# Kernel optimization log

Hardware: AMD Instinct MI355X
Metric: run time of the kernel (lower is better)

Reference implementation:

```python
import jax, jax.numpy as jnp
import numpy as np

B, S, H, E, TOP_K = 4, 4096, 4096, 64, 2

def setup_inputs() -> dict:
    key = jax.random.key(0)
    k1, k2 = jax.random.split(key)
    hidden_states = jax.random.normal(k1, (B, S, H), dtype=jnp.float32)
    gate_weight = jax.random.normal(k2, (E, H), dtype=jnp.float32) * (H ** -0.5)
    return {"hidden_states": hidden_states, "gate_weight": gate_weight}

def reference(hidden_states, gate_weight):
    # gate: logits[b,s,e] = hidden[b,s,h] @ W[e,h]^T (nn.Linear, no bias)
    router_logits = jnp.einsum('bsh,eh->bse', hidden_states, gate_weight)
    router_probs = jax.nn.softmax(router_logits, axis=-1)
    # top-k over experts, then renormalize the selected weights
    expert_weights, expert_indices = jax.lax.top_k(router_probs, TOP_K)
    expert_weights = expert_weights / jnp.sum(expert_weights, axis=-1, keepdims=True)
    return (router_probs, expert_indices, expert_weights)
```

## Files before the change

### kernel.cpp

```cpp
#include <hip/hip_runtime.h>
#include <math.h>

#define TOKENS 16384
#define HDIM 4096
#define NE 64

#define BM 128
#define BK 32
#define KSPLIT 8
#define KSLICE (HDIM / KSPLIT)

__global__ __launch_bounds__(128) void router_gemm(const float* __restrict__ A,
                                                   const float* __restrict__ W,
                                                   float* __restrict__ P) {
  __shared__ float As[BK][BM];
  __shared__ float Ws[BK][NE];

  const int tid = threadIdx.x;
  const int bt = blockIdx.x;
  const int ks = blockIdx.y;
  const int tx = tid & 7;
  const int ty = tid >> 3;

  const float* Ab = A + (size_t)(bt * BM + tid) * HDIM + (size_t)ks * KSLICE;
  const int we = tid >> 1;
  const int wk = (tid & 1) * 16;
  const float* Wb = W + (size_t)we * HDIM + (size_t)ks * KSLICE + wk;

  float acc[8][8];
#pragma unroll
  for (int i = 0; i < 8; ++i)
#pragma unroll
    for (int j = 0; j < 8; ++j) acc[i][j] = 0.f;

  for (int kc = 0; kc < KSLICE; kc += BK) {
#pragma unroll
    for (int i = 0; i < BK / 4; ++i) {
      float4 v = *(const float4*)(Ab + kc + i * 4);
      As[i * 4 + 0][tid] = v.x;
      As[i * 4 + 1][tid] = v.y;
      As[i * 4 + 2][tid] = v.z;
      As[i * 4 + 3][tid] = v.w;
    }
#pragma unroll
    for (int i = 0; i < 4; ++i) {
      float4 v = *(const float4*)(Wb + kc + i * 4);
      Ws[wk + i * 4 + 0][we] = v.x;
      Ws[wk + i * 4 + 1][we] = v.y;
      Ws[wk + i * 4 + 2][we] = v.z;
      Ws[wk + i * 4 + 3][we] = v.w;
    }
    __syncthreads();

#pragma unroll
    for (int k = 0; k < BK; ++k) {
      float a[8], w[8];
      *(float4*)&a[0] = *(const float4*)&As[k][ty * 8];
      *(float4*)&a[4] = *(const float4*)&As[k][ty * 8 + 4];
      *(float4*)&w[0] = *(const float4*)&Ws[k][tx * 8];
      *(float4*)&w[4] = *(const float4*)&Ws[k][tx * 8 + 4];
#pragma unroll
      for (int i = 0; i < 8; ++i)
#pragma unroll
        for (int j = 0; j < 8; ++j) acc[i][j] = fmaf(a[i], w[j], acc[i][j]);
    }
    __syncthreads();
  }

  float* Pb = P + ((size_t)ks * TOKENS + (size_t)bt * BM + ty * 8) * NE + tx * 8;
#pragma unroll
  for (int i = 0; i < 8; ++i) {
    float4 v0 = make_float4(acc[i][0], acc[i][1], acc[i][2], acc[i][3]);
    float4 v1 = make_float4(acc[i][4], acc[i][5], acc[i][6], acc[i][7]);
    *(float4*)(Pb + (size_t)i * NE) = v0;
    *(float4*)(Pb + (size_t)i * NE + 4) = v1;
  }
}

__global__ __launch_bounds__(64) void router_finalize(const float* __restrict__ P,
                                                      float* __restrict__ out) {
  const int tok = blockIdx.x * 64 + threadIdx.x;
  float l[NE];

#pragma unroll
  for (int j = 0; j < NE / 4; ++j) {
    float4 v = *(const float4*)(P + (size_t)tok * NE + j * 4);
    l[j * 4 + 0] = v.x; l[j * 4 + 1] = v.y; l[j * 4 + 2] = v.z; l[j * 4 + 3] = v.w;
  }
#pragma unroll
  for (int s = 1; s < KSPLIT; ++s) {
    const float* ps = P + ((size_t)s * TOKENS + tok) * NE;
#pragma unroll
    for (int j = 0; j < NE / 4; ++j) {
      float4 v = *(const float4*)(ps + j * 4);
      l[j * 4 + 0] += v.x; l[j * 4 + 1] += v.y; l[j * 4 + 2] += v.z; l[j * 4 + 3] += v.w;
    }
  }

  float m = l[0];
#pragma unroll
  for (int e = 1; e < NE; ++e) m = fmaxf(m, l[e]);
  float sum = 0.f;
#pragma unroll
  for (int e = 0; e < NE; ++e) { l[e] = expf(l[e] - m); sum += l[e]; }
  const float inv = 1.f / sum;

  float v0 = -1.f, v1 = -1.f;
  int i0 = 0, i1 = 0;
#pragma unroll
  for (int e = 0; e < NE; ++e) {
    float p = l[e] * inv;
    l[e] = p;
    if (p > v0) { v1 = v0; i1 = i0; v0 = p; i0 = e; }
    else if (p > v1) { v1 = p; i1 = e; }
  }

  float* probs = out + (size_t)tok * NE;
#pragma unroll
  for (int j = 0; j < NE / 4; ++j)
    *(float4*)(probs + j * 4) =
        make_float4(l[j * 4 + 0], l[j * 4 + 1], l[j * 4 + 2], l[j * 4 + 3]);

  float* idxo = out + (size_t)TOKENS * NE + (size_t)tok * 2;
  idxo[0] = (float)i0;
  idxo[1] = (float)i1;

  float* wo = out + (size_t)TOKENS * NE + (size_t)TOKENS * 2 + (size_t)tok * 2;
  const float rs = 1.f / (v0 + v1);
  wo[0] = v0 * rs;
  wo[1] = v1 * rs;
}

extern "C" void kernel_launch(void* const* d_in, const int* in_sizes, int n_in,
                              void* d_out, int out_size, void* d_ws, size_t ws_size,
                              hipStream_t stream) {
  const float* A = (const float*)d_in[0];
  const float* W = (const float*)d_in[1];
  float* out = (float*)d_out;
  float* P = (float*)d_ws;

  dim3 gridA(TOKENS / BM, KSPLIT);
  router_gemm<<<gridA, 128, 0, stream>>>(A, W, P);
  router_finalize<<<TOKENS / 64, 64, 0, stream>>>(P, out);
}
```

Baseline: 407.1 us.

## Retile router GEMM with register prefetch and wave-parallel softmax/top-k finalize

The GEMM moves from 128-token tiles with 8x8 per-thread outputs to 64-token tiles with 256 threads and 4x4 outputs. It pads the shared-memory arrays to reduce bank conflicts and prefetches the next K chunk into registers while the current one is computed. The finalize kernel changes from one thread per token to one wavefront per token, doing max, sum and top-2 with shuffles and ballots instead of serial loops over 64 registers. The aim is more parallelism and lower latency, at the cost of lower arithmetic intensity per thread and more LDS traffic per FMA in the GEMM.

```diff
diff --git a/kernel.cpp b/kernel.cpp
--- a/kernel.cpp
+++ b/kernel.cpp
@@ -5,130 +5,134 @@
 #define HDIM 4096
 #define NE 64
 
-#define BM 128
+#define BM 64
 #define BK 32
 #define KSPLIT 8
 #define KSLICE (HDIM / KSPLIT)
+#define LDSP 68
 
-__global__ __launch_bounds__(128) void router_gemm(const float* __restrict__ A,
-                                                   const float* __restrict__ W,
-                                                   float* __restrict__ P) {
-  __shared__ float As[BK][BM];
-  __shared__ float Ws[BK][NE];
+__global__ __launch_bounds__(256, 4) void router_gemm(const float* __restrict__ A,
+                                                      const float* __restrict__ W,
+                                                      float* __restrict__ P) {
+  __shared__ float As[BK * LDSP];
+  __shared__ float Ws[BK * LDSP];
 
   const int tid = threadIdx.x;
   const int bt = blockIdx.x;
   const int ks = blockIdx.y;
-  const int tx = tid & 7;
-  const int ty = tid >> 3;
 
-  const float* Ab = A + (size_t)(bt * BM + tid) * HDIM + (size_t)ks * KSLICE;
-  const int we = tid >> 1;
-  const int wk = (tid & 1) * 16;
-  const float* Wb = W + (size_t)we * HDIM + (size_t)ks * KSLICE + wk;
+  const int sr = tid >> 2;
+  const int sc = (tid & 3) * 4;
 
-  float acc[8][8];
+  const float* Ab = A + (size_t)(bt * BM + sr) * HDIM + (size_t)ks * KSLICE + sc;
+  const float* Wb = W + (size_t)sr * HDIM + (size_t)ks * KSLICE + sc;
+
+  const int tx = tid & 15;
+  const int ty = tid >> 4;
+
+  float acc[4][4];
 #pragma unroll
-  for (int i = 0; i < 8; ++i)
+  for (int i = 0; i < 4; ++i)
 #pragma unroll
-    for (int j = 0; j < 8; ++j) acc[i][j] = 0.f;
+    for (int j = 0; j < 4; ++j) acc[i][j] = 0.f;
+
+  float4 a0 = *(const float4*)(Ab);
+  float4 a1 = *(const float4*)(Ab + 16);
+  float4 w0 = *(const float4*)(Wb);
+  float4 w1 = *(const float4*)(Wb + 16);
 
   for (int kc = 0; kc < KSLICE; kc += BK) {
-#pragma unroll
-    for (int i = 0; i < BK / 4; ++i) {
-      float4 v = *(const float4*)(Ab + kc + i * 4);
-      As[i * 4 + 0][tid] = v.x;
-      As[i * 4 + 1][tid] = v.y;
-      As[i * 4 + 2][tid] = v.z;
-      As[i * 4 + 3][tid] = v.w;
+    As[(sc + 0) * LDSP + sr] = a0.x;
+    As[(sc + 1) * LDSP + sr] = a0.y;
+    As[(sc + 2) * LDSP + sr] = a0.z;
+    As[(sc + 3) * LDSP + sr] = a0.w;
+    As[(sc + 16) * LDSP + sr] = a1.x;
+    As[(sc + 17) * LDSP + sr] = a1.y;
+    As[(sc + 18) * LDSP + sr] = a1.z;
+    As[(sc + 19) * LDSP + sr] = a1.w;
+    Ws[(sc + 0) * LDSP + sr] = w0.x;
+    Ws[(sc + 1) * LDSP + sr] = w0.y;
+    Ws[(sc + 2) * LDSP + sr] = w0.z;
+    Ws[(sc + 3) * LDSP + sr] = w0.w;
+    Ws[(sc + 16) * LDSP + sr] = w1.x;
+    Ws[(sc + 17) * LDSP + sr] = w1.y;
+    Ws[(sc + 18) * LDSP + sr] = w1.z;
+    Ws[(sc + 19) * LDSP + sr] = w1.w;
+    __syncthreads();
+
+    if (kc + BK < KSLICE) {
+      a0 = *(const float4*)(Ab + kc + BK);
+      a1 = *(const float4*)(Ab + kc + BK + 16);
+      w0 = *(const float4*)(Wb + kc + BK);
+      w1 = *(const float4*)(Wb + kc + BK + 16);
     }
-#pragma unroll
-    for (int i = 0; i < 4; ++i) {
-      float4 v = *(const float4*)(Wb + kc + i * 4);
-      Ws[wk + i * 4 + 0][we] = v.x;
-      Ws[wk + i * 4 + 1][we] = v.y;
-      Ws[wk + i * 4 + 2][we] = v.z;
-      Ws[wk + i * 4 + 3][we] = v.w;
-    }
-    __syncthreads();
 
 #pragma unroll
     for (int k = 0; k < BK; ++k) {
-      float a[8], w[8];
-      *(float4*)&a[0] = *(const float4*)&As[k][ty * 8];
-      *(float4*)&a[4] = *(const float4*)&As[k][ty * 8 + 4];
-      *(float4*)&w[0] = *(const float4*)&Ws[k][tx * 8];
-      *(float4*)&w[4] = *(const float4*)&Ws[k][tx * 8 + 4];
+      float4 av = *(const float4*)&As[k * LDSP + ty * 4];
+      float4 wv = *(const float4*)&Ws[k * LDSP + tx * 4];
+      const float a[4] = {av.x, av.y, av.z, av.w};
+      const float w[4] = {wv.x, wv.y, wv.z, wv.w};
 #pragma unroll
-      for (int i = 0; i < 8; ++i)
+      for (int i = 0; i < 4; ++i)
 #pragma unroll
-        for (int j = 0; j < 8; ++j) acc[i][j] = fmaf(a[i], w[j], acc[i][j]);
+        for (int j = 0; j < 4; ++j) acc[i][j] = fmaf(a[i], w[j], acc[i][j]);
     }
     __syncthreads();
   }
 
-  float* Pb = P + ((size_t)ks * TOKENS + (size_t)bt * BM + ty * 8) * NE + tx * 8;
+  float* Pb = P + ((size_t)ks * TOKENS + (size_t)bt * BM + ty * 4) * NE + tx * 4;
 #pragma unroll
-  for (int i = 0; i < 8; ++i) {
-    float4 v0 = make_float4(acc[i][0], acc[i][1], acc[i][2], acc[i][3]);
-    float4 v1 = make_float4(acc[i][4], acc[i][5], acc[i][6], acc[i][7]);
-    *(float4*)(Pb + (size_t)i * NE) = v0;
-    *(float4*)(Pb + (size_t)i * NE + 4) = v1;
-  }
+  for (int i = 0; i < 4; ++i)
+    *(float4*)(Pb + (size_t)i * NE) =
+        make_float4(acc[i][0], acc[i][1], acc[i][2], acc[i][3]);
 }
 
-__global__ __launch_bounds__(64) void router_finalize(const float* __restrict__ P,
-                                                      float* __restrict__ out) {
-  const int tok = blockIdx.x * 64 + threadIdx.x;
-  float l[NE];
+__global__ __launch_bounds__(256) void router_finalize(const float* __restrict__ P,
+                                                       float* __restrict__ out) {
+  const int lane = threadIdx.x & 63;
+  const int wave = threadIdx.x >> 6;
+  const int tok = blockIdx.x * 4 + wave;
 
+  float l = 0.f;
 #pragma unroll
-  for (int j = 0; j < NE / 4; ++j) {
-    float4 v = *(const float4*)(P + (size_t)tok * NE + j * 4);
-    l[j * 4 + 0] = v.x; l[j * 4 + 1] = v.y; l[j * 4 + 2] = v.z; l[j * 4 + 3] = v.w;
+  for (int s = 0; s < KSPLIT; ++s)
+    l += P[((size_t)s * TOKENS + tok) * NE + lane];
+
+  float m = l;
+#pragma unroll
+  for (int off = 32; off >= 1; off >>= 1) m = fmaxf(m, __shfl_xor(m, off, 64));
+
+  const float e = expf(l - m);
+  float sum = e;
+#pragma unroll
+  for (int off = 32; off >= 1; off >>= 1) sum += __shfl_xor(sum, off, 64);
+
+  const float p = e / sum;
+  out[(size_t)tok * NE + lane] = p;
+
+  float m0 = p;
+#pragma unroll
+  for (int off = 32; off >= 1; off >>= 1) m0 = fmaxf(m0, __shfl_xor(m0, off, 64));
+  const unsigned long long b0 = __ballot(p == m0);
+  const int i0 = __ffsll(b0) - 1;
+
+  const float pm = (lane == i0) ? -1.f : p;
+  float m1 = pm;
+#pragma unroll
+  for (int off = 32; off >= 1; off >>= 1) m1 = fmaxf(m1, __shfl_xor(m1, off, 64));
+  const unsigned long long b1 = __ballot(pm == m1);
+  const int i1 = __ffsll(b1) - 1;
+
+  if (lane == 0) {
+    float* idxo = out + (size_t)TOKENS * NE + (size_t)tok * 2;
+    idxo[0] = (float)i0;
+    idxo[1] = (float)i1;
+    float* wo = out + (size_t)TOKENS * NE + (size_t)TOKENS * 2 + (size_t)tok * 2;
+    const float d = m0 + m1;
+    wo[0] = m0 / d;
+    wo[1] = m1 / d;
   }
-#pragma unroll
-  for (int s = 1; s < KSPLIT; ++s) {
-    const float* ps = P + ((size_t)s * TOKENS + tok) * NE;
-#pragma unroll
-    for (int j = 0; j < NE / 4; ++j) {
-      float4 v = *(const float4*)(ps + j * 4);
-      l[j * 4 + 0] += v.x; l[j * 4 + 1] += v.y; l[j * 4 + 2] += v.z; l[j * 4 + 3] += v.w;
-    }
-  }
-
-  float m = l[0];
-#pragma unroll
-  for (int e = 1; e < NE; ++e) m = fmaxf(m, l[e]);
-  float sum = 0.f;
-#pragma unroll
-  for (int e = 0; e < NE; ++e) { l[e] = expf(l[e] - m); sum += l[e]; }
-  const float inv = 1.f / sum;
-
-  float v0 = -1.f, v1 = -1.f;
-  int i0 = 0, i1 = 0;
-#pragma unroll
-  for (int e = 0; e < NE; ++e) {
-    float p = l[e] * inv;
-    l[e] = p;
-    if (p > v0) { v1 = v0; i1 = i0; v0 = p; i0 = e; }
-    else if (p > v1) { v1 = p; i1 = e; }
-  }
-
-  float* probs = out + (size_t)tok * NE;
-#pragma unroll
-  for (int j = 0; j < NE / 4; ++j)
-    *(float4*)(probs + j * 4) =
-        make_float4(l[j * 4 + 0], l[j * 4 + 1], l[j * 4 + 2], l[j * 4 + 3]);
-
-  float* idxo = out + (size_t)TOKENS * NE + (size_t)tok * 2;
-  idxo[0] = (float)i0;
-  idxo[1] = (float)i1;
-
-  float* wo = out + (size_t)TOKENS * NE + (size_t)TOKENS * 2 + (size_t)tok * 2;
-  const float rs = 1.f / (v0 + v1);
-  wo[0] = v0 * rs;
-  wo[1] = v1 * rs;
 }
 
 extern "C" void kernel_launch(void* const* d_in, const int* in_sizes, int n_in,
@@ -140,6 +144,6 @@
   float* P = (float*)d_ws;
 
   dim3 gridA(TOKENS / BM, KSPLIT);
-  router_gemm<<<gridA, 128, 0, stream>>>(A, W, P);
-  router_finalize<<<TOKENS / 64, 64, 0, stream>>>(P, out);
+  router_gemm<<<gridA, 256, 0, stream>>>(A, W, P);
+  router_finalize<<<TOKENS / 4, 256, 0, stream>>>(P, out);
 }
```

New measurement: 399.4 us. About the same (-1.9%).
